# Kernel tuning notes

Hardware: AMD Instinct MI355X
Metric: run time of the kernel (lower is better)

Reference implementation:

```python
import jax, jax.numpy as jnp
import numpy as np

EPS = 1e-12  # torch F.normalize eps

def _normalize(x):
    # L2-normalize along last dim, matching F.normalize(dim=-1)
    n = jnp.linalg.norm(x, axis=-1, keepdims=True)
    return x / jnp.maximum(n, EPS)

def setup_inputs() -> dict:
    key = jax.random.key(0)
    k1, k2, k3 = jax.random.split(key, 3)
    B, K, D = 32768, 8, 256
    return {
        "drone_slots": jax.random.normal(k1, (B, K, D), dtype=jnp.float32),
        "sat_slots": jax.random.normal(k2, (B, K, D), dtype=jnp.float32),
        "labels": jax.random.randint(k3, (B,), 0, 1000, dtype=jnp.int64),
        "temperature": 0.1,
    }

def reference(drone_slots, sat_slots, labels, temperature):
    # labels are unused by the original math (targets are arange(K))
    ds = _normalize(drone_slots)  # [B,K,D]
    ss = _normalize(sat_slots)    # [B,K,D]
    logits = jnp.einsum("bkd,bjd->bkj", ds, ss) / temperature  # [B,K,K]
    # cross_entropy with targets = arange(K): positive is the diagonal
    lse = jax.nn.logsumexp(logits, axis=-1)                      # [B,K]
    pos = jnp.diagonal(logits, axis1=-2, axis2=-1)               # [B,K]
    ce_per_sample = jnp.mean(lse - pos, axis=-1)                 # [B], per-sample mean-reduced CE
    return jnp.mean(ce_per_sample)                               # average over batch
```

## Files before the change

### kernel.cpp

```cpp
#include <hip/hip_runtime.h>
#include <hip/hip_bf16.h>


typedef __attribute__((ext_vector_type(8))) short bf16x8;
typedef __attribute__((ext_vector_type(4))) float f32x4;

union BFPack { bf16x8 v; __hip_bfloat162 h[4]; };

__device__ inline bf16x8 pack8(const float4& lo, const float4& hi) {
  BFPack u;
  u.h[0] = __float22bfloat162_rn(make_float2(lo.x, lo.y));
  u.h[1] = __float22bfloat162_rn(make_float2(lo.z, lo.w));
  u.h[2] = __float22bfloat162_rn(make_float2(hi.x, hi.y));
  u.h[3] = __float22bfloat162_rn(make_float2(hi.z, hi.w));
  return u.v;
}

extern "C" __global__ __launch_bounds__(256)
void slot_ce_mfma(const float* __restrict__ ds, const float* __restrict__ ss,
                  const float* __restrict__ tptr, float* __restrict__ ws,
                  int ntiles) {
  const int lane = threadIdx.x & 63;
  const int wid  = blockIdx.x * 4 + (threadIdx.x >> 6);
  const int m = lane & 15;
  const int h = lane >> 4;
  const float inv_t = 1.0f / tptr[0];

  float loss = 0.0f;

  if (wid < ntiles) {
    const float4* pa = (const float4*)(ds + (size_t)wid * 4096);
    const float4* pb = (const float4*)(ss + (size_t)wid * 4096);
    const int base = m * 64 + h;

    f32x4 acc = {0.f, 0.f, 0.f, 0.f};
    float ssqA = 0.f, ssqS = 0.f;

#pragma unroll
    for (int kb = 0; kb < 8; ++kb) {
      const int i0 = base + kb * 8;
      float4 a0 = pa[i0], a1 = pa[i0 + 4];
      float4 s0 = pb[i0], s1 = pb[i0 + 4];

      ssqA += a0.x*a0.x + a0.y*a0.y + a0.z*a0.z + a0.w*a0.w
            + a1.x*a1.x + a1.y*a1.y + a1.z*a1.z + a1.w*a1.w;
      ssqS += s0.x*s0.x + s0.y*s0.y + s0.z*s0.z + s0.w*s0.w
            + s1.x*s1.x + s1.y*s1.y + s1.z*s1.z + s1.w*s1.w;

      acc = __builtin_amdgcn_mfma_f32_16x16x32_bf16(
          pack8(a0, a1), pack8(s0, s1), acc, 0, 0, 0);
    }

    ssqA += __shfl_xor(ssqA, 16, 64);
    ssqA += __shfl_xor(ssqA, 32, 64);
    ssqS += __shfl_xor(ssqS, 16, 64);
    ssqS += __shfl_xor(ssqS, 32, 64);
    float na0 = __shfl(ssqA, h * 4 + 0, 64);
    float na1 = __shfl(ssqA, h * 4 + 1, 64);
    float na2 = __shfl(ssqA, h * 4 + 2, 64);
    float na3 = __shfl(ssqA, h * 4 + 3, 64);

    float lg0 = acc[0] * rsqrtf(na0 * ssqS) * inv_t;
    float lg1 = acc[1] * rsqrtf(na1 * ssqS) * inv_t;
    float lg2 = acc[2] * rsqrtf(na2 * ssqS) * inv_t;
    float lg3 = acc[3] * rsqrtf(na3 * ssqS) * inv_t;

    float c = 0.0f;
#pragma unroll
    for (int r = 0; r < 4; ++r) {
      float lg = r == 0 ? lg0 : r == 1 ? lg1 : r == 2 ? lg2 : lg3;
      float mx = lg;
      mx = fmaxf(mx, __shfl_xor(mx, 1, 64));
      mx = fmaxf(mx, __shfl_xor(mx, 2, 64));
      mx = fmaxf(mx, __shfl_xor(mx, 4, 64));
      float e = __expf(lg - mx);
      e += __shfl_xor(e, 1, 64);
      e += __shfl_xor(e, 2, 64);
      e += __shfl_xor(e, 4, 64);
      float lse = mx + __logf(e);
      c += lse * 0.125f;
      if (4 * h + r == m) c -= lg;
    }
    if ((m >= 8) == (h >= 2)) loss = c;
  }

#pragma unroll
  for (int o = 32; o >= 1; o >>= 1) loss += __shfl_xor(loss, o, 64);
  __shared__ float red[4];
  if (lane == 0) red[threadIdx.x >> 6] = loss;
  __syncthreads();
  if (threadIdx.x == 0)
    ws[blockIdx.x] = (red[0] + red[1]) + (red[2] + red[3]);
}

extern "C" __global__ __launch_bounds__(256)
void slot_ce_finish(const float* __restrict__ ws, float* __restrict__ out,
                    int nparts, float scale) {
  __shared__ float red[256];
  float s = 0.0f;
  for (int i = threadIdx.x; i < nparts; i += 256) s += ws[i];
  red[threadIdx.x] = s;
  __syncthreads();
  for (int o = 128; o >= 1; o >>= 1) {
    if ((int)threadIdx.x < o) red[threadIdx.x] += red[threadIdx.x + o];
    __syncthreads();
  }
  if (threadIdx.x == 0) out[0] = red[0] * scale;
}

extern "C" void kernel_launch(void* const* d_in, const int* in_sizes, int n_in,
                              void* d_out, int out_size, void* d_ws, size_t ws_size,
                              hipStream_t stream) {
  const float* ds   = (const float*)d_in[0];
  const float* ss   = (const float*)d_in[1];
  const float* tptr = (const float*)d_in[3];
  float* out = (float*)d_out;
  float* ws  = (float*)d_ws;

  const int B      = in_sizes[0] / (8 * 256);
  const int ntiles = B / 2;
  const int blocks = (ntiles + 3) / 4;

  slot_ce_mfma<<<blocks, 256, 0, stream>>>(ds, ss, tptr, ws, ntiles);
  const float scale = 1.0f / (8.0f * (float)B);
  slot_ce_finish<<<1, 256, 0, stream>>>(ws, out, blocks, scale);
}
```

Measured before the change: 101.5 us.

## Fuse final reduction via last-block atomic counter and software-pipeline loads

Merges the finish kernel into the main kernel: each block writes its partial sum, bumps an atomic counter, and the last block to arrive reduces all partials and writes the output. A hipMemsetAsync resets the counter each call. The k-loop is also hand-unrolled with double-buffered register loads and sched_barriers so the next loads are issued before the current MFMA step. This removes one kernel launch and its gap, but adds a memset node and relies on the fence and counter protocol being correct.

```diff
diff --git a/kernel.cpp b/kernel.cpp
--- a/kernel.cpp
+++ b/kernel.cpp
@@ -16,12 +16,32 @@
   return u.v;
 }
 
+__device__ inline void step(const float4& a0, const float4& a1,
+                            const float4& s0, const float4& s1,
+                            float& ssqA, float& ssqS, f32x4& acc) {
+  ssqA += a0.x*a0.x + a0.y*a0.y + a0.z*a0.z + a0.w*a0.w
+        + a1.x*a1.x + a1.y*a1.y + a1.z*a1.z + a1.w*a1.w;
+  ssqS += s0.x*s0.x + s0.y*s0.y + s0.z*s0.z + s0.w*s0.w
+        + s1.x*s1.x + s1.y*s1.y + s1.z*s1.z + s1.w*s1.w;
+  acc = __builtin_amdgcn_mfma_f32_16x16x32_bf16(
+      pack8(a0, a1), pack8(s0, s1), acc, 0, 0, 0);
+}
+
+#define LOADK(B, KB)                                                     \
+  aA##B = pa[base + (KB) * 8];  aB##B = pa[base + (KB) * 8 + 4];         \
+  sA##B = pb[base + (KB) * 8];  sB##B = pb[base + (KB) * 8 + 4];
+
+#define SB __builtin_amdgcn_sched_barrier(0)
+
 extern "C" __global__ __launch_bounds__(256)
-void slot_ce_mfma(const float* __restrict__ ds, const float* __restrict__ ss,
-                  const float* __restrict__ tptr, float* __restrict__ ws,
-                  int ntiles) {
-  const int lane = threadIdx.x & 63;
-  const int wid  = blockIdx.x * 4 + (threadIdx.x >> 6);
+void slot_ce_fused(const float* __restrict__ ds, const float* __restrict__ ss,
+                   const float* __restrict__ tptr, float* __restrict__ ws,
+                   unsigned* __restrict__ counter, float* __restrict__ out,
+                   int ntiles, int nblocks, float scale) {
+  const int tid  = threadIdx.x;
+  const int lane = tid & 63;
+  const int wv   = tid >> 6;
+  const int wid  = blockIdx.x * 4 + wv;
   const int m = lane & 15;
   const int h = lane >> 4;
   const float inv_t = 1.0f / tptr[0];
@@ -36,20 +56,16 @@
     f32x4 acc = {0.f, 0.f, 0.f, 0.f};
     float ssqA = 0.f, ssqS = 0.f;
 
-#pragma unroll
-    for (int kb = 0; kb < 8; ++kb) {
-      const int i0 = base + kb * 8;
-      float4 a0 = pa[i0], a1 = pa[i0 + 4];
-      float4 s0 = pb[i0], s1 = pb[i0 + 4];
-
-      ssqA += a0.x*a0.x + a0.y*a0.y + a0.z*a0.z + a0.w*a0.w
-            + a1.x*a1.x + a1.y*a1.y + a1.z*a1.z + a1.w*a1.w;
-      ssqS += s0.x*s0.x + s0.y*s0.y + s0.z*s0.z + s0.w*s0.w
-            + s1.x*s1.x + s1.y*s1.y + s1.z*s1.z + s1.w*s1.w;
-
-      acc = __builtin_amdgcn_mfma_f32_16x16x32_bf16(
-          pack8(a0, a1), pack8(s0, s1), acc, 0, 0, 0);
-    }
+    float4 aA0, aB0, sA0, sB0, aA1, aB1, sA1, sB1;
+    LOADK(0, 0); LOADK(1, 1); SB;
+    step(aA0, aB0, sA0, sB0, ssqA, ssqS, acc); LOADK(0, 2); SB;
+    step(aA1, aB1, sA1, sB1, ssqA, ssqS, acc); LOADK(1, 3); SB;
+    step(aA0, aB0, sA0, sB0, ssqA, ssqS, acc); LOADK(0, 4); SB;
+    step(aA1, aB1, sA1, sB1, ssqA, ssqS, acc); LOADK(1, 5); SB;
+    step(aA0, aB0, sA0, sB0, ssqA, ssqS, acc); LOADK(0, 6); SB;
+    step(aA1, aB1, sA1, sB1, ssqA, ssqS, acc); LOADK(1, 7); SB;
+    step(aA0, aB0, sA0, sB0, ssqA, ssqS, acc);
+    step(aA1, aB1, sA1, sB1, ssqA, ssqS, acc);
 
     ssqA += __shfl_xor(ssqA, 16, 64);
     ssqA += __shfl_xor(ssqA, 32, 64);
@@ -86,26 +102,32 @@
 
 #pragma unroll
   for (int o = 32; o >= 1; o >>= 1) loss += __shfl_xor(loss, o, 64);
-  __shared__ float red[4];
-  if (lane == 0) red[threadIdx.x >> 6] = loss;
+  __shared__ float sred[256];
+  __shared__ unsigned sflag;
+  if (lane == 0) sred[wv] = loss;
   __syncthreads();
-  if (threadIdx.x == 0)
-    ws[blockIdx.x] = (red[0] + red[1]) + (red[2] + red[3]);
-}
+  if (tid == 0) {
+    const float part = (sred[0] + sred[1]) + (sred[2] + sred[3]);
+    atomicExch(&ws[blockIdx.x], part);
+    __threadfence();
+    const unsigned old = atomicAdd(counter, 1u);
+    sflag = (old == (unsigned)(nblocks - 1)) ? 1u : 0u;
+  }
+  __syncthreads();
 
-extern "C" __global__ __launch_bounds__(256)
-void slot_ce_finish(const float* __restrict__ ws, float* __restrict__ out,
-                    int nparts, float scale) {
-  __shared__ float red[256];
-  float s = 0.0f;
-  for (int i = threadIdx.x; i < nparts; i += 256) s += ws[i];
-  red[threadIdx.x] = s;
-  __syncthreads();
-  for (int o = 128; o >= 1; o >>= 1) {
-    if ((int)threadIdx.x < o) red[threadIdx.x] += red[threadIdx.x + o];
+  if (sflag) {
+    __threadfence();
+    float s = 0.0f;
+    for (int i = tid; i < nblocks; i += 256)
+      s += ((volatile float*)ws)[i];
+    sred[tid] = s;
     __syncthreads();
+    for (int o = 128; o >= 1; o >>= 1) {
+      if (tid < o) sred[tid] += sred[tid + o];
+      __syncthreads();
+    }
+    if (tid == 0) out[0] = sred[0] * scale;
   }
-  if (threadIdx.x == 0) out[0] = red[0] * scale;
 }
 
 extern "C" void kernel_launch(void* const* d_in, const int* in_sizes, int n_in,
@@ -116,12 +138,14 @@
   const float* tptr = (const float*)d_in[3];
   float* out = (float*)d_out;
   float* ws  = (float*)d_ws;
+  unsigned* counter = (unsigned*)((char*)d_ws + 16384);
 
-  const int B      = in_sizes[0] / (8 * 256);
-  const int ntiles = B / 2;
-  const int blocks = (ntiles + 3) / 4;
+  const int B       = in_sizes[0] / (8 * 256);
+  const int ntiles  = B / 2;
+  const int nblocks = (ntiles + 3) / 4;
 
-  slot_ce_mfma<<<blocks, 256, 0, stream>>>(ds, ss, tptr, ws, ntiles);
+  hipMemsetAsync(counter, 0, sizeof(unsigned), stream);
   const float scale = 1.0f / (8.0f * (float)B);
-  slot_ce_finish<<<1, 256, 0, stream>>>(ws, out, blocks, scale);
+  slot_ce_fused<<<nblocks, 256, 0, stream>>>(ds, ss, tptr, ws, counter, out,
+                                             ntiles, nblocks, scale);
 }
```

Result: slower. 306.4 us (+201.7%).
